# Kernel tuning notes

Hardware: AMD Instinct MI355X
Metric: run time of the kernel (lower is better)

The kernel has to match this reference:

```python
import jax, jax.numpy as jnp
import numpy as np

LANDMARKS = 80
POINT_LANDMARKS = tuple(range(468, 538))  # 70 hand-region indices
AVG_SET = [[0,40],[40,40],[80,60],[140,60],[200,60],[260,60],[320,50],[370,50],[420,60],[480,63]]
STAT_CAP = 168


def nan_mean(x, axis=0):
    m = jnp.isnan(x)
    num = jnp.where(m, 0.0, x).sum(axis)
    den = jnp.where(m, 0.0, 1.0).sum(axis)
    return num / den


def nan_std(x, axis=0):
    d = x - nan_mean(x, axis=axis)
    return jnp.sqrt(nan_mean(d * d, axis=axis))


def flatten_means_and_stds(x, reshape1):
    # x: [t, L, C] -> stats over frames -> [2L, C] -> (1, reshape1*2)
    out = jnp.concatenate([nan_mean(x, 0), nan_std(x, 0)], axis=0)
    if out.shape[0] > STAT_CAP:
        out = out[:STAT_CAP, :]
    out = out.reshape(1, reshape1 * 2)
    return jnp.where(jnp.isfinite(out), out, jnp.zeros_like(out))


def setup_inputs() -> dict:
    key = jax.random.key(0)
    T, N, C = 32768, 543, 3
    x_in = jax.random.normal(key, (T, N, C), dtype=jnp.float32)
    return {
        "x_in": x_in,
        "num_frames": 16384,
        "segments": 4,
        "input_shape": (16384, 240),
    }


def reference(x_in, num_frames, segments, input_shape):
    # 1) cluster means + point gather -> x: [T, LANDMARKS, 3]
    parts = [jnp.mean(x_in[:, s:s + l, :], axis=1, keepdims=True) for s, l in AVG_SET]
    parts.append(x_in[:, jnp.array(POINT_LANDMARKS), :])
    x = jnp.concatenate(parts, axis=1)

    # 2) symmetric padding loop (axis 1), gated on T % segments as in the original
    xp = x
    rem = x.shape[0] % segments  # shapes are static -> Python int
    for i in range(segments):
        p0 = 1 if (rem > 0 and i % 2 != 0) else 0
        p1 = 1 if (rem > 0 and i % 2 == 0) else 0
        if p0 or p1:
            xp = jnp.pad(xp, ((0, 0), (p0, p1), (0, 0)), mode='symmetric')

    # 3) per-segment nan mean/std stats
    segs = np.array_split(np.arange(xp.shape[0]), segments)
    feats = [flatten_means_and_stds(xp[idx[0]:idx[-1] + 1], input_shape[1]) for idx in segs]
    feats.append(flatten_means_and_stds(x, input_shape[1]))

    # 4) bilinear resize (align_corners=False semantics, no antialias)
    xi = jnp.transpose(x, (2, 0, 1))[None]            # [1, 3, T, L]
    xi = jax.image.resize(xi, (1, 3, num_frames, LANDMARKS), method='bilinear', antialias=False)
    xi = jnp.transpose(xi[0], (1, 2, 0))              # [num_frames, L, 3]
    xi = xi.reshape(1, input_shape[0] * input_shape[1])
    xi = jnp.where(jnp.isnan(xi), jnp.zeros_like(xi), xi)
    feats.append(xi)

    return jnp.concatenate(feats, axis=1)
```

## Files before the change

### kernel.cpp

```cpp
#include <hip/hip_runtime.h>
#include <math.h>

#define T_FRAMES   32768
#define N_LM       543
#define FRAME      1629
#define FPB        32
#define NBLOCKS    (T_FRAMES / FPB)
#define OUT_B_OFF  2400
#define ACC_FLOATS 1920

__constant__ int   c_astart[10] = {0, 40, 80, 140, 200, 260, 320, 370, 420, 480};
__constant__ int   c_alen[10]   = {40, 40, 60, 60, 60, 60, 50, 50, 60, 63};

__global__ void zero_acc_kernel(float* __restrict__ acc) {
    int i = blockIdx.x * 256 + threadIdx.x;
    if (i < ACC_FLOATS) acc[i] = 0.0f;
}

__global__ __launch_bounds__(256) void featgen_main(
    const float* __restrict__ xin, float* __restrict__ out, float* __restrict__ acc)
{
    __shared__ float rows[4 * FRAME];
    __shared__ float xavg[4 * 32];

    const int t = threadIdx.x;
    const int b = blockIdx.x;
    const float* src = xin + (size_t)b * (FPB * FRAME);

    const int g8 = t >> 3;
    const int j8 = t & 7;
    int a_s = 0, a_n = 0, a_c = 0;
    float a_inv = 0.0f;
    if (g8 < 30) {
        int l = g8 / 3; a_c = g8 - 3 * l;
        a_s = c_astart[l]; a_n = c_alen[l];
        a_inv = 1.0f / (float)a_n;
    }

    float ssum = 0.0f, ssq = 0.0f;

    for (int grp = 0; grp < 8; ++grp) {
        const float4* s4 = (const float4*)(src + grp * (4 * FRAME));
        float4* d4 = (float4*)rows;
        #pragma unroll
        for (int i = 0; i < 7; ++i) {
            int idx = t + i * 256;
            if (idx < FRAME) d4[idx] = s4[idx];
        }
        __syncthreads();

        if (g8 < 30) {
            #pragma unroll
            for (int f = 0; f < 4; ++f) {
                const float* row = rows + f * FRAME;
                float s = 0.0f;
                for (int j = j8; j < a_n; j += 8) s += row[(a_s + j) * 3 + a_c];
                s += __shfl_xor(s, 1, 8);
                s += __shfl_xor(s, 2, 8);
                s += __shfl_xor(s, 4, 8);
                if (j8 == 0) xavg[f * 32 + g8] = s * a_inv;
            }
        }
        __syncthreads();

        if (t < 240) {
            float v0, v1, v2, v3;
            if (t < 30) {
                v0 = xavg[0 * 32 + t]; v1 = xavg[1 * 32 + t];
                v2 = xavg[2 * 32 + t]; v3 = xavg[3 * 32 + t];
            } else {
                v0 = rows[0 * FRAME + t + 1374];
                v1 = rows[1 * FRAME + t + 1374];
                v2 = rows[2 * FRAME + t + 1374];
                v3 = rows[3 * FRAME + t + 1374];
            }
            const size_t row0 = (size_t)b * 16 + (size_t)grp * 2;
            out[OUT_B_OFF + row0 * 240 + t]       = 0.5f * (v0 + v1);
            out[OUT_B_OFF + (row0 + 1) * 240 + t] = 0.5f * (v2 + v3);
            ssum += v0 + v1 + v2 + v3;
            ssq  += v0 * v0 + v1 * v1 + v2 * v2 + v3 * v3;
        }
        __syncthreads();
    }

    if (t < 240) {
        const int seg = b >> 8;
        atomicAdd(&acc[seg * 480 + t],       ssum);
        atomicAdd(&acc[seg * 480 + 240 + t], ssq);
    }
}

__global__ __launch_bounds__(256) void finalize_stats(
    const float* __restrict__ acc, float* __restrict__ out)
{
    const int f = blockIdx.x;
    const int t = threadIdx.x;
    if (t >= 240) return;
    float s, q, n;
    if (f < 4) {
        s = acc[f * 480 + t];
        q = acc[f * 480 + 240 + t];
        n = 8192.0f;
    } else {
        s = acc[t]       + acc[480 + t]  + acc[960 + t]  + acc[1440 + t];
        q = acc[240 + t] + acc[720 + t]  + acc[1200 + t] + acc[1680 + t];
        n = 32768.0f;
    }
    float mean = s / n;
    float var  = q / n - mean * mean;
    var = var < 0.0f ? 0.0f : var;
    out[f * 480 + t]       = mean;
    out[f * 480 + 240 + t] = sqrtf(var);
}

extern "C" void kernel_launch(void* const* d_in, const int* in_sizes, int n_in,
                              void* d_out, int out_size, void* d_ws, size_t ws_size,
                              hipStream_t stream) {
    (void)in_sizes; (void)n_in; (void)out_size; (void)ws_size;
    const float* xin = (const float*)d_in[0];
    float* out = (float*)d_out;
    float* acc = (float*)d_ws;

    zero_acc_kernel<<<8, 256, 0, stream>>>(acc);
    featgen_main<<<NBLOCKS, 256, 0, stream>>>(xin, out, acc);
    finalize_stats<<<5, 256, 0, stream>>>(acc, out);
}
```

Before: 309.1 us.

## Halve frames per block and replace atomic stat accumulation with partial-sum reduction

```diff
diff --git a/kernel.cpp b/kernel.cpp
--- a/kernel.cpp
+++ b/kernel.cpp
@@ -2,26 +2,21 @@
 #include <math.h>
 
 #define T_FRAMES   32768
-#define N_LM       543
 #define FRAME      1629
-#define FPB        32
+#define FPB        16
 #define NBLOCKS    (T_FRAMES / FPB)
 #define OUT_B_OFF  2400
-#define ACC_FLOATS 1920
+#define SEG_BLOCKS (NBLOCKS / 4)
+#define MID_OFF    ((size_t)NBLOCKS * 480)
 
-__constant__ int   c_astart[10] = {0, 40, 80, 140, 200, 260, 320, 370, 420, 480};
-__constant__ int   c_alen[10]   = {40, 40, 60, 60, 60, 60, 50, 50, 60, 63};
-
-__global__ void zero_acc_kernel(float* __restrict__ acc) {
-    int i = blockIdx.x * 256 + threadIdx.x;
-    if (i < ACC_FLOATS) acc[i] = 0.0f;
-}
+__constant__ int c_astart[10] = {0, 40, 80, 140, 200, 260, 320, 370, 420, 480};
+__constant__ int c_alen[10]   = {40, 40, 60, 60, 60, 60, 50, 50, 60, 63};
 
 __global__ __launch_bounds__(256) void featgen_main(
-    const float* __restrict__ xin, float* __restrict__ out, float* __restrict__ acc)
+    const float* __restrict__ xin, float* __restrict__ out, float* __restrict__ part)
 {
-    __shared__ float rows[4 * FRAME];
-    __shared__ float xavg[4 * 32];
+    __shared__ float rows[2 * FRAME];
+    __shared__ float xavg[2 * 32];
 
     const int t = threadIdx.x;
     const int b = blockIdx.x;
@@ -39,19 +34,19 @@
 
     float ssum = 0.0f, ssq = 0.0f;
 
-    for (int grp = 0; grp < 8; ++grp) {
-        const float4* s4 = (const float4*)(src + grp * (4 * FRAME));
-        float4* d4 = (float4*)rows;
+    for (int u = 0; u < 8; ++u) {
+        const float2* s2 = (const float2*)(src + u * (2 * FRAME));
+        float2* d2 = (float2*)rows;
         #pragma unroll
         for (int i = 0; i < 7; ++i) {
             int idx = t + i * 256;
-            if (idx < FRAME) d4[idx] = s4[idx];
+            if (idx < FRAME) d2[idx] = s2[idx];
         }
         __syncthreads();
 
         if (g8 < 30) {
             #pragma unroll
-            for (int f = 0; f < 4; ++f) {
+            for (int f = 0; f < 2; ++f) {
                 const float* row = rows + f * FRAME;
                 float s = 0.0f;
                 for (int j = j8; j < a_n; j += 8) s += row[(a_s + j) * 3 + a_c];
@@ -64,46 +59,61 @@
         __syncthreads();
 
         if (t < 240) {
-            float v0, v1, v2, v3;
+            float v0, v1;
             if (t < 30) {
-                v0 = xavg[0 * 32 + t]; v1 = xavg[1 * 32 + t];
-                v2 = xavg[2 * 32 + t]; v3 = xavg[3 * 32 + t];
+                v0 = xavg[t]; v1 = xavg[32 + t];
             } else {
-                v0 = rows[0 * FRAME + t + 1374];
-                v1 = rows[1 * FRAME + t + 1374];
-                v2 = rows[2 * FRAME + t + 1374];
-                v3 = rows[3 * FRAME + t + 1374];
+                v0 = rows[t + 1374];
+                v1 = rows[FRAME + t + 1374];
             }
-            const size_t row0 = (size_t)b * 16 + (size_t)grp * 2;
-            out[OUT_B_OFF + row0 * 240 + t]       = 0.5f * (v0 + v1);
-            out[OUT_B_OFF + (row0 + 1) * 240 + t] = 0.5f * (v2 + v3);
-            ssum += v0 + v1 + v2 + v3;
-            ssq  += v0 * v0 + v1 * v1 + v2 * v2 + v3 * v3;
+            out[OUT_B_OFF + ((size_t)b * 8 + u) * 240 + t] = 0.5f * (v0 + v1);
+            ssum += v0 + v1;
+            ssq  += v0 * v0 + v1 * v1;
         }
         __syncthreads();
     }
 
     if (t < 240) {
-        const int seg = b >> 8;
-        atomicAdd(&acc[seg * 480 + t],       ssum);
-        atomicAdd(&acc[seg * 480 + 240 + t], ssq);
+        part[(size_t)b * 480 + t]       = ssum;
+        part[(size_t)b * 480 + 240 + t] = ssq;
     }
 }
 
+__global__ __launch_bounds__(512) void reduce_parts(
+    const float* __restrict__ part, float* __restrict__ mid)
+{
+    const int f = blockIdx.x >> 2;
+    const int c = blockIdx.x & 3;
+    const int t = threadIdx.x;
+    if (t >= 480) return;
+    const int b0 = f * SEG_BLOCKS + c * (SEG_BLOCKS / 4);
+    float s = 0.0f;
+    #pragma unroll 4
+    for (int b = 0; b < SEG_BLOCKS / 4; ++b)
+        s += part[(size_t)(b0 + b) * 480 + t];
+    mid[(size_t)blockIdx.x * 480 + t] = s;
+}
+
 __global__ __launch_bounds__(256) void finalize_stats(
-    const float* __restrict__ acc, float* __restrict__ out)
+    const float* __restrict__ mid, float* __restrict__ out)
 {
     const int f = blockIdx.x;
     const int t = threadIdx.x;
     if (t >= 240) return;
-    float s, q, n;
+    float s = 0.0f, q = 0.0f, n;
     if (f < 4) {
-        s = acc[f * 480 + t];
-        q = acc[f * 480 + 240 + t];
+        #pragma unroll
+        for (int c = 0; c < 4; ++c) {
+            s += mid[(size_t)(f * 4 + c) * 480 + t];
+            q += mid[(size_t)(f * 4 + c) * 480 + 240 + t];
+        }
         n = 8192.0f;
     } else {
-        s = acc[t]       + acc[480 + t]  + acc[960 + t]  + acc[1440 + t];
-        q = acc[240 + t] + acc[720 + t]  + acc[1200 + t] + acc[1680 + t];
+        #pragma unroll
+        for (int m = 0; m < 16; ++m) {
+            s += mid[(size_t)m * 480 + t];
+            q += mid[(size_t)m * 480 + 240 + t];
+        }
         n = 32768.0f;
     }
     float mean = s / n;
@@ -118,10 +128,11 @@
                               hipStream_t stream) {
     (void)in_sizes; (void)n_in; (void)out_size; (void)ws_size;
     const float* xin = (const float*)d_in[0];
-    float* out = (float*)d_out;
-    float* acc = (float*)d_ws;
+    float* out  = (float*)d_out;
+    float* part = (float*)d_ws;
+    float* mid  = part + MID_OFF;
 
-    zero_acc_kernel<<<8, 256, 0, stream>>>(acc);
-    featgen_main<<<NBLOCKS, 256, 0, stream>>>(xin, out, acc);
-    finalize_stats<<<5, 256, 0, stream>>>(acc, out);
+    featgen_main<<<NBLOCKS, 256, 0, stream>>>(xin, out, part);
+    reduce_parts<<<16, 512, 0, stream>>>(part, mid);
+    finalize_stats<<<5, 256, 0, stream>>>(mid, out);
 }
```

Result: slower. 318.9 us (+3.2%).
